# Optimization experiments

Hardware: AMD Instinct MI355X
Metric: run time of the kernel (lower is better)

The kernel has to match this reference:

```python
import jax, jax.numpy as jnp
import numpy as np

HID = 1024
HEADS = 16
HEAD_DIM = HID // HEADS
PF = 4096
EPS = 1e-5


def _linear_params(key, d_in, d_out):
    kw, kb = jax.random.split(key)
    bound = 1.0 / np.sqrt(d_in)
    W = jax.random.uniform(kw, (d_in, d_out), jnp.float32, -bound, bound)
    b = jax.random.uniform(kb, (d_out,), jnp.float32, -bound, bound)
    return W, b


def setup_inputs() -> dict:
    key = jax.random.key(0)
    ks = jax.random.split(key, 8)
    src = jax.random.normal(ks[0], (4, 2048, HID), jnp.float32)
    src_mask = jnp.ones((4, 1, 1, 2048), jnp.int32)
    Wq, bq = _linear_params(ks[1], HID, HID)
    Wk, bk = _linear_params(ks[2], HID, HID)
    Wv, bv = _linear_params(ks[3], HID, HID)
    Wo, bo = _linear_params(ks[4], HID, HID)
    W1, b1 = _linear_params(ks[5], HID, PF)
    W2, b2 = _linear_params(ks[6], PF, HID)
    ln1_g = jnp.ones((HID,), jnp.float32); ln1_b = jnp.zeros((HID,), jnp.float32)
    ln2_g = jnp.ones((HID,), jnp.float32); ln2_b = jnp.zeros((HID,), jnp.float32)
    return dict(src=src, src_mask=src_mask, Wq=Wq, bq=bq, Wk=Wk, bk=bk,
                Wv=Wv, bv=bv, Wo=Wo, bo=bo, W1=W1, b1=b1, W2=W2, b2=b2,
                ln1_g=ln1_g, ln1_b=ln1_b, ln2_g=ln2_g, ln2_b=ln2_b)


def _layernorm(x, g, b):
    mu = jnp.mean(x, axis=-1, keepdims=True)
    var = jnp.mean(jnp.square(x - mu), axis=-1, keepdims=True)
    return (x - mu) * jax.lax.rsqrt(var + EPS) * g + b


def _forward(src, src_mask, Wq, bq, Wk, bk, Wv, bv, Wo, bo,
             W1, b1, W2, b2, ln1_g, ln1_b, ln2_g, ln2_b):
    B, S, _ = src.shape
    # multi-head attention
    Q = (src @ Wq + bq).reshape(B, S, HEADS, HEAD_DIM)
    K = (src @ Wk + bk).reshape(B, S, HEADS, HEAD_DIM)
    V = (src @ Wv + bv).reshape(B, S, HEADS, HEAD_DIM)
    scale = np.sqrt(HEAD_DIM).astype(np.float32)
    energy = jnp.einsum('bqnh,bknh->bnqk', Q, K) / scale
    energy = jnp.where(src_mask == 0, jnp.float32(-1e10), energy)
    attn = jax.nn.softmax(energy, axis=-1)
    x = jnp.einsum('bnqk,bknh->bqnh', attn, V).reshape(B, S, HID)
    x = x @ Wo + bo
    src = _layernorm(src + x, ln1_g, ln1_b)
    # feedforward (swish)
    h = src @ W1 + b1
    h = h * jax.nn.sigmoid(h)
    h = h @ W2 + b2
    return _layernorm(src + h, ln2_g, ln2_b)


def reference(src, src_mask, Wq, bq, Wk, bk, Wv, bv, Wo, bo,
              W1, b1, W2, b2, ln1_g, ln1_b, ln2_g, ln2_b):
    return _forward(src, src_mask, Wq, bq, Wk, bk, Wv, bv, Wo, bo,
                    W1, b1, W2, b2, ln1_g, ln1_b, ln2_g, ln2_b)
```

## Files before the change

kernel.cpp:

```cpp
#include <hip/hip_runtime.h>
#include <stdint.h>


typedef __bf16 bf16;
typedef __bf16 bf16x4 __attribute__((ext_vector_type(4)));
typedef __bf16 bf16x8 __attribute__((ext_vector_type(8)));
typedef float  f32x4  __attribute__((ext_vector_type(4)));

__device__ __forceinline__ bf16 f2b(float x){
  uint32_t u = __builtin_bit_cast(uint32_t, x);
  uint32_t r = (u + 0x7FFFu + ((u >> 16) & 1u)) >> 16;
  return __builtin_bit_cast(bf16, (uint16_t)r);
}

__device__ __forceinline__ float ex2(float x){
#if __has_builtin(__builtin_amdgcn_exp2f)
  return __builtin_amdgcn_exp2f(x);
#else
  return __exp2f(x);
#endif
}

__device__ __forceinline__ void gload_lds16(const void* g, void* l){
  __builtin_amdgcn_global_load_lds(
      (const __attribute__((address_space(1))) void*)g,
      (__attribute__((address_space(3))) void*)l, 16, 0, 0);
}

__global__ __launch_bounds__(256) void prep_kernel(
    const float* __restrict__ src, bf16* __restrict__ srcb,
    const float* __restrict__ Wq, const float* __restrict__ Wk,
    const float* __restrict__ Wv, const float* __restrict__ Wo,
    const float* __restrict__ W1, const float* __restrict__ W2,
    bf16* __restrict__ Wqkvt, bf16* __restrict__ Wot,
    bf16* __restrict__ W1t,  bf16* __restrict__ W2t)
{
  __shared__ float t[32][33];
  const int bb = blockIdx.x, tid = threadIdx.x;
  if (bb < 8192){
    const int i = bb*256 + tid;
    const float4 v = ((const float4*)src)[i];
    bf16x4 u = { f2b(v.x), f2b(v.y), f2b(v.z), f2b(v.w) };
    *(bf16x4*)(srcb + (size_t)i*4) = u;
    return;
  }
  const int idx = bb - 8192;
  const float* W; bf16* Wt; int K, N, bx, by;
  if (idx < 3072){
    const int r = idx >> 10, j = idx & 1023;
    W = (r==0)?Wq:(r==1)?Wk:Wv; Wt = Wqkvt + (size_t)r*1024*1024;
    K = 1024; N = 1024; bx = j & 31; by = j >> 5;
  } else if (idx < 4096){
    const int j = idx - 3072;
    W = Wo; Wt = Wot; K = 1024; N = 1024; bx = j & 31; by = j >> 5;
  } else if (idx < 8192){
    const int j = idx - 4096;
    W = W1; Wt = W1t; K = 1024; N = 4096; bx = j & 127; by = j >> 7;
  } else {
    const int j = idx - 8192;
    W = W2; Wt = W2t; K = 4096; N = 1024; bx = j & 31; by = j >> 5;
  }
  const int x = tid & 31, y = tid >> 5;
  const int n0 = bx*32, k0 = by*32;
  #pragma unroll
  for (int r=0;r<4;r++) t[y+8*r][x] = W[(size_t)(k0+y+8*r)*N + n0+x];
  __syncthreads();
  #pragma unroll
  for (int r=0;r<4;r++) Wt[(size_t)(n0+y+8*r)*K + k0+x] = f2b(t[x][y+8*r]);
}

template<int OMODE, int REMAP>
__global__ __launch_bounds__(256) void gemm_bt_kernel(
    const bf16* __restrict__ A, const bf16* __restrict__ Bt,
    const float* __restrict__ bias, void* __restrict__ C,
    int M, int N, int K, float oscale,
    const float* __restrict__ bias2, const float* __restrict__ bias3,
    void* __restrict__ C2, void* __restrict__ C3)
{
  __shared__ bf16 As[128*64];
  __shared__ bf16 Bs[128*64];
  const int tid = threadIdx.x;
  const int w = tid >> 6, lane = tid & 63;
  const int wr = w >> 1, wc = w & 1;
  const int g16 = lane >> 4, l16 = lane & 15;

  const int nbx = N >> 7;
  const int nby = M >> 7;
  const int lin = blockIdx.x;
  int bx, by;
  if constexpr (REMAP==1){
    const int xcd = lin & 7;
    const int j   = lin >> 3;
    by = xcd * (nby >> 3) + (j / nbx);
    bx = j % nbx;
  } else {
    bx = lin % nbx;
    by = lin / nbx;
  }
  const int m0 = by*128, n0 = bx*128;

  const int srow  = tid >> 3;
  const int sslot = ((tid & 7) ^ (srow & 7)) * 8;
  const bf16* gA = A  + (size_t)(m0 + srow)*K + sslot;
  const bf16* gB = Bt + (size_t)(n0 + srow)*K + sslot;

  f32x4 acc[4][4];
  const f32x4 fz = {0.f,0.f,0.f,0.f};
  #pragma unroll
  for (int m=0;m<4;m++)
    #pragma unroll
    for (int n=0;n<4;n++) acc[m][n] = fz;

  bf16x8 ra[4], rb[4];
  #pragma unroll
  for (int k=0;k<4;k++){
    ra[k] = *(const bf16x8*)(gA + (size_t)(32*k)*K);
    rb[k] = *(const bf16x8*)(gB + (size_t)(32*k)*K);
  }

  const int l7 = l16 & 7;
  for (int k0=0; k0<K; k0+=64){
    __syncthreads();
    #pragma unroll
    for (int k=0;k<4;k++){
      *(bf16x8*)&As[(tid + 256*k)*8] = ra[k];
      *(bf16x8*)&Bs[(tid + 256*k)*8] = rb[k];
    }
    __syncthreads();
    if (k0 + 64 < K){
      #pragma unroll
      for (int k=0;k<4;k++){
        ra[k] = *(const bf16x8*)(gA + (size_t)(32*k)*K + k0 + 64);
        rb[k] = *(const bf16x8*)(gB + (size_t)(32*k)*K + k0 + 64);
      }
    }
    #pragma unroll
    for (int kk=0;kk<2;kk++){
      bf16x8 af[4], bfv[4];
      #pragma unroll
      for (int m=0;m<4;m++){
        const int r = wr*64 + m*16 + l16;
        af[m] = *(const bf16x8*)&As[r*64 + ((((kk<<2)+g16) ^ l7)<<3)];
      }
      #pragma unroll
      for (int n=0;n<4;n++){
        const int r = wc*64 + n*16 + l16;
        bfv[n] = *(const bf16x8*)&Bs[r*64 + ((((kk<<2)+g16) ^ l7)<<3)];
      }
      #pragma unroll
      for (int m=0;m<4;m++)
        #pragma unroll
        for (int n=0;n<4;n++)
          acc[m][n] = __builtin_amdgcn_mfma_f32_16x16x32_bf16(af[m], bfv[n], acc[m][n], 0, 0, 0);
    }
  }

  const int cb = n0 + wc*64 + l16;
  if constexpr (OMODE==4){
    const int region = n0 >> 10;
    const float* bs = (region==0)? bias : (region==1)? bias2 : bias3;
    const int colbase = region << 10;
    #pragma unroll
    for (int n=0;n<4;n++){
      const int cl = cb + n*16 - colbase;
      const float bv = bs[cl];
      #pragma unroll
      for (int m=0;m<4;m++){
        const int rbase = m0 + wr*64 + m*16 + g16*4;
        if (region==2){
          const size_t bq = (size_t)rbase >> 11;
          const int s  = rbase & 2047;
          const int s6 = s & 63;
          const int sp = (s & ~63) | (s6 & 32) | ((s6 & 12) << 1)
                       | ((s6 & 16) >> 2);
          bf16x4 v4 = { f2b(acc[m][n][0] + bv), f2b(acc[m][n][1] + bv),
                        f2b(acc[m][n][2] + bv), f2b(acc[m][n][3] + bv) };
          *(bf16x4*)&((bf16*)C3)[(bq*1024 + (size_t)cl)*2048 + sp] = v4;
        } else {
          #pragma unroll
          for (int r=0;r<4;r++){
            const float v = acc[m][n][r] + bv;
            const size_t row = (size_t)(rbase + r);
            if (region==0) ((bf16*)C )[row*1024 + cl] = f2b(v * oscale);
            else           ((bf16*)C2)[row*1024 + cl] = f2b(v);
          }
        }
      }
    }
  } else {
    #pragma unroll
    for (int n=0;n<4;n++){
      const int col = cb + n*16;
      const float bv = bias[col];
      #pragma unroll
      for (int m=0;m<4;m++){
        const int rbase = m0 + wr*64 + m*16 + g16*4;
        #pragma unroll
        for (int r=0;r<4;r++){
          float v = acc[m][n][r] + bv;
          const size_t row = (size_t)(rbase + r);
          if constexpr (OMODE==0){
            ((float*)C)[row*N + col] = v;
          } else if constexpr (OMODE==1){
            ((bf16*)C)[row*N + col] = f2b(v * oscale);
          } else {
            v = v / (1.f + __expf(-v));
            ((bf16*)C)[row*N + col] = f2b(v);
          }
        }
      }
    }
  }
}

__global__ __launch_bounds__(512) void attn_kernel(
    const bf16* __restrict__ Q, const bf16* __restrict__ Km,
    const bf16* __restrict__ Vt, const int* __restrict__ msk,
    bf16* __restrict__ O)
{
  __shared__ bf16 Ks[3][64*64];
  __shared__ bf16 Vs[3][64*64];
  __shared__ int  Mflag[32];

  const int tid = threadIdx.x;
  const int w = tid>>6, lane = tid&63;
  const int g16 = lane>>4, l16 = lane&15;
  const int lin = blockIdx.x;
  const int xcd = lin & 7, idx = lin >> 3;
  const int bh  = xcd*8 + (idx >> 3);
  const int qt  = idx & 7;
  const int b = bh >> 4, h = bh & 15;
  const int q0 = qt*256 + w*32;

  const bf16* Kb = Km + (size_t)b*2048*1024 + h*64;
  const bf16* Vb = Vt + (size_t)(b*16 + h)*64*2048;
  const int*  mb = msk + b*2048;

  if (tid < 32) Mflag[tid] = 1;

  const int srow = w*8 + (lane>>3);
  const int sslot = ((lane&7) ^ (lane>>3)) * 8;
  const bf16* gK0 = Kb + (size_t)srow*1024 + sslot;
  const bf16* gV0 = Vb + (size_t)srow*2048 + sslot;

  auto stage = [&](int buf, int kv0){
    gload_lds16(gK0 + (size_t)kv0*1024, &Ks[buf][w*512]);
    gload_lds16(gV0 + kv0,              &Vs[buf][w*512]);
  };

  bf16x8 qf[2][2];
  #pragma unroll
  for (int qg=0;qg<2;qg++){
    const bf16* qp = Q + (size_t)(b*2048 + q0 + qg*16 + l16)*1024 + h*64 + g16*8;
    qf[qg][0] = *(const bf16x8*)qp;
    qf[qg][1] = *(const bf16x8*)(qp + 32);
  }

  __syncthreads();
  {
    const int4 a = *(const int4*)(mb + tid*4);
    const bool ok = a.x && a.y && a.z && a.w;
    if (!ok) atomicAnd(&Mflag[tid>>4], 0);
  }
  stage(0, 0);
  stage(1, 64);
  __syncthreads();

  const int l7 = l16 & 7;
  const int kOff0 = l16*64 + ((g16     ^ l7) << 3);
  const int kOff1 = l16*64 + (((4+g16) ^ l7) << 3);

  bf16x8 ones8;
  #pragma unroll
  for (int j=0;j<8;j++) ones8[j] = (bf16)1.0f;

  const f32x4 fz = {0.f,0.f,0.f,0.f};
  f32x4 xa[2][4];
  f32x4 lacc[2] = {fz, fz};
  #pragma unroll
  for (int qg=0;qg<2;qg++)
    #pragma unroll
    for (int jd=0;jd<4;jd++) xa[qg][jd] = fz;

  int cur = 0;
  for (int it = 0; it < 32; ++it){
    const int kv0 = it*64;
    const bf16* ksb = &Ks[cur][0];
    const bf16* vsb = &Vs[cur][0];

    bf16x8 kk[4][2];
    #pragma unroll
    for (int t=0;t<4;t++){
      kk[t][0] = *(const bf16x8*)(ksb + t*1024 + kOff0);
      kk[t][1] = *(const bf16x8*)(ksb + t*1024 + kOff1);
    }
    bf16x8 vw[2][4];
    #pragma unroll
    for (int jd=0;jd<4;jd++){
      vw[0][jd] = *(const bf16x8*)(vsb + jd*1024 + kOff0);
      vw[1][jd] = *(const bf16x8*)(vsb + jd*1024 + kOff1);
    }

    if (it < 30){
      const int pb = (cur >= 1) ? cur-1 : 2;
      stage(pb, kv0 + 128);
    }
    if (it < 30)       asm volatile("s_waitcnt vmcnt(2)" ::: "memory");
    else if (it == 30) asm volatile("s_waitcnt vmcnt(0)" ::: "memory");
    if (it < 31){
      asm volatile("" ::: "memory");
      __builtin_amdgcn_s_barrier();
      asm volatile("" ::: "memory");
    }

    f32x4 st[2][4];
    __builtin_amdgcn_s_setprio(1);
    #pragma unroll
    for (int qg=0;qg<2;qg++){
      #pragma unroll
      for (int t=0;t<4;t++){
        f32x4 a = fz;
        a = __builtin_amdgcn_mfma_f32_16x16x32_bf16(kk[t][0], qf[qg][0], a, 0,0,0);
        a = __builtin_amdgcn_mfma_f32_16x16x32_bf16(kk[t][1], qf[qg][1], a, 0,0,0);
        st[qg][t] = a;
      }
    }
    __builtin_amdgcn_s_setprio(0);

    if (!Mflag[it]){
      int4 mm[4];
      #pragma unroll
      for (int t=0;t<4;t++) mm[t] = *(const int4*)(mb + kv0 + t*16 + 4*g16);
      #pragma unroll
      for (int qg=0;qg<2;qg++)
        #pragma unroll
        for (int t=0;t<4;t++){
          st[qg][t][0] = (mm[t].x==0) ? -1e9f : st[qg][t][0];
          st[qg][t][1] = (mm[t].y==0) ? -1e9f : st[qg][t][1];
          st[qg][t][2] = (mm[t].z==0) ? -1e9f : st[qg][t][2];
          st[qg][t][3] = (mm[t].w==0) ? -1e9f : st[qg][t][3];
        }
    }

    bf16x8 pw[2][2];
    #pragma unroll
    for (int qg=0;qg<2;qg++){
      #pragma unroll
      for (int t=0;t<4;t++){
        const int hb = (t&1)*4;
        pw[qg][t>>1][hb+0] = (bf16)ex2(st[qg][t][0]);
        pw[qg][t>>1][hb+1] = (bf16)ex2(st[qg][t][1]);
        pw[qg][t>>1][hb+2] = (bf16)ex2(st[qg][t][2]);
        pw[qg][t>>1][hb+3] = (bf16)ex2(st[qg][t][3]);
      }
    }
    __builtin_amdgcn_s_setprio(1);
    #pragma unroll
    for (int w2=0;w2<2;w2++){
      #pragma unroll
      for (int jd=0;jd<4;jd++){
        xa[0][jd] = __builtin_amdgcn_mfma_f32_16x16x32_bf16(vw[w2][jd], pw[0][w2], xa[0][jd], 0,0,0);
        xa[1][jd] = __builtin_amdgcn_mfma_f32_16x16x32_bf16(vw[w2][jd], pw[1][w2], xa[1][jd], 0,0,0);
      }
      lacc[0] = __builtin_amdgcn_mfma_f32_16x16x32_bf16(ones8, pw[0][w2], lacc[0], 0,0,0);
      lacc[1] = __builtin_amdgcn_mfma_f32_16x16x32_bf16(ones8, pw[1][w2], lacc[1], 0,0,0);
    }
    __builtin_amdgcn_s_setprio(0);

    cur = (cur==2) ? 0 : cur+1;
  }

  #pragma unroll
  for (int qg=0;qg<2;qg++){
    const float rl = 1.f / lacc[qg][0];
    const size_t row = (size_t)(b*2048 + q0 + qg*16 + l16);
    #pragma unroll
    for (int jd=0;jd<4;jd++){
      bf16x4 ov = { f2b(xa[qg][jd][0]*rl), f2b(xa[qg][jd][1]*rl),
                    f2b(xa[qg][jd][2]*rl), f2b(xa[qg][jd][3]*rl) };
      *(bf16x4*)(O + row*1024 + h*64 + jd*16 + 4*g16) = ov;
    }
  }
}

template<int RBF>
__global__ __launch_bounds__(256) void addln_kernel(
    const bf16* __restrict__ X, const void* __restrict__ R,
    const float* __restrict__ g, const float* __restrict__ be,
    float* __restrict__ of, bf16* __restrict__ ob)
{
  const int row = blockIdx.x, tid = threadIdx.x;
  const bf16x4 vxb = *(const bf16x4*)(X + (size_t)row*1024 + tid*4);
  float r0, r1, r2, r3;
  if constexpr (RBF==1){
    const bf16x4 vrb = *(const bf16x4*)((const bf16*)R + (size_t)row*1024 + tid*4);
    r0 = (float)vrb[0]; r1 = (float)vrb[1]; r2 = (float)vrb[2]; r3 = (float)vrb[3];
  } else {
    const float4 vr = ((const float4*)((const float*)R + (size_t)row*1024))[tid];
    r0 = vr.x; r1 = vr.y; r2 = vr.z; r3 = vr.w;
  }
  const float a0 = (float)vxb[0]+r0, a1 = (float)vxb[1]+r1;
  const float a2 = (float)vxb[2]+r2, a3 = (float)vxb[3]+r3;
  float s = a0+a1+a2+a3;
  float q = a0*a0 + a1*a1 + a2*a2 + a3*a3;
  #pragma unroll
  for (int off=1; off<64; off<<=1){
    s += __shfl_xor(s, off, 64);
    q += __shfl_xor(q, off, 64);
  }
  __shared__ float sb[8];
  if ((tid&63)==0){ sb[tid>>6] = s; sb[4+(tid>>6)] = q; }
  __syncthreads();
  s = sb[0]+sb[1]+sb[2]+sb[3];
  q = sb[4]+sb[5]+sb[6]+sb[7];
  const float mu = s*(1.f/1024.f);
  const float rs = rsqrtf(q*(1.f/1024.f) - mu*mu + 1e-5f);
  const float4 gg = ((const float4*)g)[tid];
  const float4 bb = ((const float4*)be)[tid];
  const float o0 = (a0-mu)*rs*gg.x + bb.x;
  const float o1 = (a1-mu)*rs*gg.y + bb.y;
  const float o2 = (a2-mu)*rs*gg.z + bb.z;
  const float o3 = (a3-mu)*rs*gg.w + bb.w;
  if (of){
    float4 o; o.x=o0; o.y=o1; o.z=o2; o.w=o3;
    ((float4*)(of + (size_t)row*1024))[tid] = o;
  }
  if (ob){
    bf16x4 u = { f2b(o0), f2b(o1), f2b(o2), f2b(o3) };
    *(bf16x4*)(ob + (size_t)row*1024 + tid*4) = u;
  }
}

extern "C" void kernel_launch(void* const* d_in, const int* in_sizes, int n_in,
                              void* d_out, int out_size, void* d_ws, size_t ws_size,
                              hipStream_t stream)
{
  const float* src  = (const float*)d_in[0];
  const int*   mask = (const int*)  d_in[1];
  const float* Wq = (const float*)d_in[2];  const float* bq = (const float*)d_in[3];
  const float* Wk = (const float*)d_in[4];  const float* bk = (const float*)d_in[5];
  const float* Wv = (const float*)d_in[6];  const float* bv = (const float*)d_in[7];
  const float* Wo = (const float*)d_in[8];  const float* bo = (const float*)d_in[9];
  const float* W1 = (const float*)d_in[10]; const float* b1 = (const float*)d_in[11];
  const float* W2 = (const float*)d_in[12]; const float* b2 = (const float*)d_in[13];
  const float* g1 = (const float*)d_in[14]; const float* be1 = (const float*)d_in[15];
  const float* g2 = (const float*)d_in[16]; const float* be2 = (const float*)d_in[17];

  char* ws = (char*)d_ws;
  const size_t MB = 1u<<20;
  bf16* srcb  = (bf16*)(ws + 0*MB);
  bf16* Wqkvt = (bf16*)(ws + 16*MB);
  bf16* Wot   = (bf16*)(ws + 22*MB);
  bf16* W1t   = (bf16*)(ws + 24*MB);
  bf16* W2t   = (bf16*)(ws + 32*MB);
  bf16* Qb    = (bf16*)(ws + 40*MB);
  bf16* Kb    = (bf16*)(ws + 56*MB);
  bf16* Vtb   = (bf16*)(ws + 72*MB);
  bf16* AO    = (bf16*)(ws + 88*MB);
  bf16*  X1   = (bf16*)(ws + 40*MB);
  bf16*  S1B  = (bf16*)(ws + 72*MB);
  bf16*  H1   = (bf16*)(ws + 104*MB);
  bf16*  F2   = (bf16*)(ws + 40*MB);

  const float QSC = 0.18033688011112042f;

  prep_kernel<<<20480, 256, 0, stream>>>(src, srcb, Wq, Wk, Wv, Wo, W1, W2,
                                         Wqkvt, Wot, W1t, W2t);

  gemm_bt_kernel<4,0><<<24*64, 256, 0, stream>>>(
      srcb, Wqkvt, bq, Qb, 8192, 3072, 1024, QSC, bk, bv, Kb, Vtb);

  attn_kernel<<<512, 512, 0, stream>>>(Qb, Kb, Vtb, mask, AO);

  gemm_bt_kernel<1,1><<<8*64,  256, 0, stream>>>(
      AO, Wot, bo, X1, 8192, 1024, 1024, 1.f, nullptr, nullptr, nullptr, nullptr);
  addln_kernel<0><<<8192, 256, 0, stream>>>(X1, src, g1, be1,
                                            (float*)nullptr, S1B);

  gemm_bt_kernel<2,0><<<32*64, 256, 0, stream>>>(
      S1B, W1t, b1, H1, 8192, 4096, 1024, 1.f, nullptr, nullptr, nullptr, nullptr);
  gemm_bt_kernel<1,1><<<8*64,  256, 0, stream>>>(
      H1,  W2t, b2, F2, 8192, 1024, 4096, 1.f, nullptr, nullptr, nullptr, nullptr);
  addln_kernel<1><<<8192, 256, 0, stream>>>(F2, S1B, g2, be2,
                                            (float*)d_out, (bf16*)nullptr);
}
```

Baseline: 383.1 us.

## Use triple-buffered direct global-to-LDS loads in the GEMM main loop

Replaces the register-staged, double-barrier GEMM k-loop with a 3-stage LDS ring filled by direct global_load_lds instructions, using BK=32 tiles and one barrier per iteration. The goal is to overlap global memory fetches with MFMA work and cut register pressure and LDS store instructions. It also adds an explicit lgkmcnt wait before the barrier in the attention kernel. The trade-off is twice as many loop iterations, each with a barrier, and dependence on correct vmcnt accounting.

```diff
diff --git a/kernel.cpp b/kernel.cpp
--- a/kernel.cpp
+++ b/kernel.cpp
@@ -77,8 +77,8 @@
     const float* __restrict__ bias2, const float* __restrict__ bias3,
     void* __restrict__ C2, void* __restrict__ C3)
 {
-  __shared__ bf16 As[128*64];
-  __shared__ bf16 Bs[128*64];
+  __shared__ bf16 As[3][128*32];
+  __shared__ bf16 Bs[3][128*32];
   const int tid = threadIdx.x;
   const int w = tid >> 6, lane = tid & 63;
   const int wr = w >> 1, wc = w & 1;
@@ -99,10 +99,25 @@
   }
   const int m0 = by*128, n0 = bx*128;
 
-  const int srow  = tid >> 3;
-  const int sslot = ((tid & 7) ^ (srow & 7)) * 8;
-  const bf16* gA = A  + (size_t)(m0 + srow)*K + sslot;
-  const bf16* gB = Bt + (size_t)(n0 + srow)*K + sslot;
+  const int srow  = lane >> 2;
+  const int sslot = ((lane & 3) ^ ((lane >> 3) & 3)) * 8;
+  const bf16* gA0 = A  + (size_t)(m0 + w*32      + srow)*K + sslot;
+  const bf16* gA1 = gA0 + (size_t)16*K;
+  const bf16* gB0 = Bt + (size_t)(n0 + w*32      + srow)*K + sslot;
+  const bf16* gB1 = gB0 + (size_t)16*K;
+  bf16* lA0base[3]; bf16* lB0base[3];
+  #pragma unroll
+  for (int buf=0; buf<3; ++buf){
+    lA0base[buf] = &As[buf][(2*w)*512];
+    lB0base[buf] = &Bs[buf][(2*w)*512];
+  }
+
+  auto stage = [&](int buf, int k0){
+    gload_lds16(gA0 + k0, lA0base[buf]);
+    gload_lds16(gA1 + k0, lA0base[buf] + 512);
+    gload_lds16(gB0 + k0, lB0base[buf]);
+    gload_lds16(gB1 + k0, lB0base[buf] + 512);
+  };
 
   f32x4 acc[4][4];
   const f32x4 fz = {0.f,0.f,0.f,0.f};
@@ -111,59 +126,58 @@
     #pragma unroll
     for (int n=0;n<4;n++) acc[m][n] = fz;
 
-  bf16x8 ra[4], rb[4];
-  #pragma unroll
-  for (int k=0;k<4;k++){
-    ra[k] = *(const bf16x8*)(gA + (size_t)(32*k)*K);
-    rb[k] = *(const bf16x8*)(gB + (size_t)(32*k)*K);
-  }
-
-  const int l7 = l16 & 7;
-  for (int k0=0; k0<K; k0+=64){
-    __syncthreads();
-    #pragma unroll
-    for (int k=0;k<4;k++){
-      *(bf16x8*)&As[(tid + 256*k)*8] = ra[k];
-      *(bf16x8*)&Bs[(tid + 256*k)*8] = rb[k];
-    }
-    __syncthreads();
-    if (k0 + 64 < K){
-      #pragma unroll
-      for (int k=0;k<4;k++){
-        ra[k] = *(const bf16x8*)(gA + (size_t)(32*k)*K + k0 + 64);
-        rb[k] = *(const bf16x8*)(gB + (size_t)(32*k)*K + k0 + 64);
-      }
-    }
-    #pragma unroll
-    for (int kk=0;kk<2;kk++){
-      bf16x8 af[4], bfv[4];
-      #pragma unroll
-      for (int m=0;m<4;m++){
-        const int r = wr*64 + m*16 + l16;
-        af[m] = *(const bf16x8*)&As[r*64 + ((((kk<<2)+g16) ^ l7)<<3)];
-      }
-      #pragma unroll
-      for (int n=0;n<4;n++){
-        const int r = wc*64 + n*16 + l16;
-        bfv[n] = *(const bf16x8*)&Bs[r*64 + ((((kk<<2)+g16) ^ l7)<<3)];
-      }
-      #pragma unroll
-      for (int m=0;m<4;m++)
-        #pragma unroll
-        for (int n=0;n<4;n++)
-          acc[m][n] = __builtin_amdgcn_mfma_f32_16x16x32_bf16(af[m], bfv[n], acc[m][n], 0, 0, 0);
-    }
+  const int NT = K >> 5;
+  stage(0, 0);
+  stage(1, 32);
+  asm volatile("s_waitcnt vmcnt(4)" ::: "memory");
+  __builtin_amdgcn_s_barrier();
+  asm volatile("" ::: "memory");
+
+  int cur = 0;
+  for (int t = 0; t < NT; ++t){
+    const bf16* as = &As[cur][0];
+    const bf16* bs = &Bs[cur][0];
+    bf16x8 af[4], bfv[4];
+    #pragma unroll
+    for (int m=0;m<4;m++){
+      const int r = wr*64 + m*16 + l16;
+      af[m] = *(const bf16x8*)&as[r*32 + ((g16 ^ ((r>>1)&3))<<3)];
+    }
+    #pragma unroll
+    for (int n=0;n<4;n++){
+      const int r = wc*64 + n*16 + l16;
+      bfv[n] = *(const bf16x8*)&bs[r*32 + ((g16 ^ ((r>>1)&3))<<3)];
+    }
+    if (t+2 < NT){
+      const int pb = (cur >= 1) ? cur-1 : 2;
+      stage(pb, (t+2)*32);
+      asm volatile("s_waitcnt vmcnt(4)" ::: "memory");
+    } else if (t+1 < NT){
+      asm volatile("s_waitcnt vmcnt(0)" ::: "memory");
+    }
+    asm volatile("s_waitcnt lgkmcnt(0)" ::: "memory");
+    if (t+1 < NT){
+      asm volatile("" ::: "memory");
+      __builtin_amdgcn_s_barrier();
+      asm volatile("" ::: "memory");
+    }
+    #pragma unroll
+    for (int m=0;m<4;m++)
+      #pragma unroll
+      for (int n=0;n<4;n++)
+        acc[m][n] = __builtin_amdgcn_mfma_f32_16x16x32_bf16(af[m], bfv[n], acc[m][n], 0, 0, 0);
+    cur = (cur==2) ? 0 : cur+1;
   }
 
   const int cb = n0 + wc*64 + l16;
   if constexpr (OMODE==4){
     const int region = n0 >> 10;
-    const float* bs = (region==0)? bias : (region==1)? bias2 : bias3;
+    const float* bs2 = (region==0)? bias : (region==1)? bias2 : bias3;
     const int colbase = region << 10;
     #pragma unroll
     for (int n=0;n<4;n++){
       const int cl = cb + n*16 - colbase;
-      const float bv = bs[cl];
+      const float bv = bs2[cl];
       #pragma unroll
       for (int m=0;m<4;m++){
         const int rbase = m0 + wr*64 + m*16 + g16*4;
@@ -307,6 +321,7 @@
     }
     if (it < 30)       asm volatile("s_waitcnt vmcnt(2)" ::: "memory");
     else if (it == 30) asm volatile("s_waitcnt vmcnt(0)" ::: "memory");
+    asm volatile("s_waitcnt lgkmcnt(0)" ::: "memory");
     if (it < 31){
       asm volatile("" ::: "memory");
       __builtin_amdgcn_s_barrier();
```

After: 382.4 us. Within noise of the previous version (-0.2%).

## Double-buffer LDS tiles in GEMM to drop one barrier per k-step

Applied to the files above, without the earlier changes.

The GEMM kernel now keeps two LDS buffers for the A and B tiles. Each k-iteration reads its fragments from the current buffer, then writes the already-prefetched registers into the other buffer and issues the next global loads before running the MFMAs. This cuts the two barriers per iteration down to one and overlaps LDS writes with compute. The cost is double the LDS footprint (64KB per block), which may lower occupancy; an extra lgkmcnt wait is also added before the barrier in the attention kernel.

```diff
diff --git a/kernel.cpp b/kernel.cpp
--- a/kernel.cpp
+++ b/kernel.cpp
@@ -77,8 +77,8 @@
     const float* __restrict__ bias2, const float* __restrict__ bias3,
     void* __restrict__ C2, void* __restrict__ C3)
 {
-  __shared__ bf16 As[128*64];
-  __shared__ bf16 Bs[128*64];
+  __shared__ bf16 As[2][128*64];
+  __shared__ bf16 Bs[2][128*64];
   const int tid = threadIdx.x;
   const int w = tid >> 6, lane = tid & 63;
   const int wr = w >> 1, wc = w & 1;
@@ -117,53 +117,79 @@
     ra[k] = *(const bf16x8*)(gA + (size_t)(32*k)*K);
     rb[k] = *(const bf16x8*)(gB + (size_t)(32*k)*K);
   }
+  asm volatile("s_waitcnt vmcnt(0)" ::: "memory");
+  #pragma unroll
+  for (int k=0;k<4;k++){
+    *(bf16x8*)&As[0][(tid + 256*k)*8] = ra[k];
+    *(bf16x8*)&Bs[0][(tid + 256*k)*8] = rb[k];
+  }
+  const int NT = K >> 6;
+  if (NT > 1){
+    #pragma unroll
+    for (int k=0;k<4;k++){
+      ra[k] = *(const bf16x8*)(gA + (size_t)(32*k)*K + 64);
+      rb[k] = *(const bf16x8*)(gB + (size_t)(32*k)*K + 64);
+    }
+  }
 
   const int l7 = l16 & 7;
-  for (int k0=0; k0<K; k0+=64){
-    __syncthreads();
-    #pragma unroll
-    for (int k=0;k<4;k++){
-      *(bf16x8*)&As[(tid + 256*k)*8] = ra[k];
-      *(bf16x8*)&Bs[(tid + 256*k)*8] = rb[k];
-    }
-    __syncthreads();
-    if (k0 + 64 < K){
-      #pragma unroll
-      for (int k=0;k<4;k++){
-        ra[k] = *(const bf16x8*)(gA + (size_t)(32*k)*K + k0 + 64);
-        rb[k] = *(const bf16x8*)(gB + (size_t)(32*k)*K + k0 + 64);
-      }
-    }
+  for (int t = 0; t < NT; ++t){
+    asm volatile("s_waitcnt lgkmcnt(0)" ::: "memory");
+    __builtin_amdgcn_s_barrier();
+    asm volatile("" ::: "memory");
+
+    const bf16* as = &As[t&1][0];
+    const bf16* bs = &Bs[t&1][0];
+    bf16x8 af[2][4], bfv[2][4];
     #pragma unroll
     for (int kk=0;kk<2;kk++){
-      bf16x8 af[4], bfv[4];
       #pragma unroll
       for (int m=0;m<4;m++){
         const int r = wr*64 + m*16 + l16;
-        af[m] = *(const bf16x8*)&As[r*64 + ((((kk<<2)+g16) ^ l7)<<3)];
+        af[kk][m] = *(const bf16x8*)&as[r*64 + ((((kk<<2)+g16) ^ l7)<<3)];
       }
       #pragma unroll
       for (int n=0;n<4;n++){
         const int r = wc*64 + n*16 + l16;
-        bfv[n] = *(const bf16x8*)&Bs[r*64 + ((((kk<<2)+g16) ^ l7)<<3)];
-      }
+        bfv[kk][n] = *(const bf16x8*)&bs[r*64 + ((((kk<<2)+g16) ^ l7)<<3)];
+      }
+    }
+    if (t+1 < NT){
+      asm volatile("s_waitcnt vmcnt(0)" ::: "memory");
+      bf16* aw = &As[(t+1)&1][0];
+      bf16* bw = &Bs[(t+1)&1][0];
+      #pragma unroll
+      for (int k=0;k<4;k++){
+        *(bf16x8*)&aw[(tid + 256*k)*8] = ra[k];
+        *(bf16x8*)&bw[(tid + 256*k)*8] = rb[k];
+      }
+      if (t+2 < NT){
+        #pragma unroll
+        for (int k=0;k<4;k++){
+          ra[k] = *(const bf16x8*)(gA + (size_t)(32*k)*K + (t+2)*64);
+          rb[k] = *(const bf16x8*)(gB + (size_t)(32*k)*K + (t+2)*64);
+        }
+      }
+    }
+    #pragma unroll
+    for (int kk=0;kk<2;kk++)
       #pragma unroll
       for (int m=0;m<4;m++)
         #pragma unroll
         for (int n=0;n<4;n++)
-          acc[m][n] = __builtin_amdgcn_mfma_f32_16x16x32_bf16(af[m], bfv[n], acc[m][n], 0, 0, 0);
-    }
+          acc[m][n] = __builtin_amdgcn_mfma_f32_16x16x32_bf16(
+              af[kk][m], bfv[kk][n], acc[m][n], 0, 0, 0);
   }
 
   const int cb = n0 + wc*64 + l16;
   if constexpr (OMODE==4){
     const int region = n0 >> 10;
-    const float* bs = (region==0)? bias : (region==1)? bias2 : bias3;
+    const float* bs2 = (region==0)? bias : (region==1)? bias2 : bias3;
     const int colbase = region << 10;
     #pragma unroll
     for (int n=0;n<4;n++){
       const int cl = cb + n*16 - colbase;
-      const float bv = bs[cl];
+      const float bv = bs2[cl];
       #pragma unroll
       for (int m=0;m<4;m++){
         const int rbase = m0 + wr*64 + m*16 + g16*4;
@@ -307,6 +333,7 @@
     }
     if (it < 30)       asm volatile("s_waitcnt vmcnt(2)" ::: "memory");
     else if (it == 30) asm volatile("s_waitcnt vmcnt(0)" ::: "memory");
+    asm volatile("s_waitcnt lgkmcnt(0)" ::: "memory");
     if (it < 31){
       asm volatile("" ::: "memory");
       __builtin_amdgcn_s_barrier();
```

Result: faster. 368.1 us, median of 2 (-3.9%).
